# Optimization experiments

Measured on AMD Instinct MI355X. Metric: run time of the kernel, lower is better.

The kernel has to match this reference:

```python
import jax, jax.numpy as jnp
import numpy as np

D_MODEL, NUM_HEADS, ROPE_DIM = 256, 8, 16
B_GRAPHS, N_MAX = 16, 512


def _make_batch():
    # ragged graph sizes between 256 and 512 atoms; contiguous, sorted ids
    sizes = np.array([256 + (i * 256) // 15 for i in range(B_GRAPHS)], dtype=np.int64)
    return np.repeat(np.arange(B_GRAPHS), sizes)  # total N = 6137


def setup_inputs() -> dict:
    key = jax.random.key(0)
    ks = jax.random.split(key, 6)
    batch_np = _make_batch()
    N = int(batch_np.shape[0])
    x = jax.random.normal(ks[0], (N, D_MODEL), jnp.float32)
    pos = jax.random.normal(ks[1], (N, 3), jnp.float32) * 3.0
    W_qkv = jax.random.normal(ks[2], (D_MODEL, 3 * D_MODEL), jnp.float32) / np.sqrt(D_MODEL).astype(np.float32)
    W_out = jax.random.normal(ks[3], (D_MODEL, D_MODEL), jnp.float32) / np.sqrt(D_MODEL).astype(np.float32)
    rope_freqs = jax.random.normal(ks[4], (ROPE_DIM,), jnp.float32) * 0.1
    W_rope = jax.random.normal(ks[5], (ROPE_DIM, NUM_HEADS), jnp.float32) / np.sqrt(ROPE_DIM).astype(np.float32)
    gamma = jnp.ones((D_MODEL,), jnp.float32)
    beta = jnp.zeros((D_MODEL,), jnp.float32)
    return {"x": x, "pos": pos, "batch": jnp.asarray(batch_np, jnp.int32),
            "W_qkv": W_qkv, "W_out": W_out, "rope_freqs": rope_freqs,
            "W_rope": W_rope, "gamma": gamma, "beta": beta,
            "B": B_GRAPHS, "n_max": N_MAX}


def _forward(x, pos, W_qkv, W_out, rope_freqs, W_rope, gamma, beta, batch, B, n_max):
    N, d = x.shape
    H = W_rope.shape[1]
    hd = d // H
    scale = hd ** -0.5
    # pad ragged graphs to [B, n_max] via vectorized scatter (batch is sorted)
    sizes = jax.ops.segment_sum(jnp.ones((N,), jnp.int32), batch, num_segments=B)
    offsets = jnp.concatenate([jnp.zeros((1,), jnp.int32), jnp.cumsum(sizes)[:-1].astype(jnp.int32)])
    pidx = jnp.arange(N, dtype=jnp.int32) - offsets[batch]  # position within graph
    x_pad = jnp.zeros((B, n_max, d), x.dtype).at[batch, pidx].set(x)
    pos_pad = jnp.zeros((B, n_max, 3), pos.dtype).at[batch, pidx].set(pos)
    pad = jnp.ones((B, n_max), bool).at[batch, pidx].set(False)  # True = padding
    # multi-head self-attention on scalar channel
    qkv = x_pad @ W_qkv  # [B, n, 3d]
    q, k, v = jnp.split(qkv, 3, axis=-1)
    heads = lambda t: t.reshape(B, n_max, H, hd).transpose(0, 2, 1, 3)  # [B,H,n,hd]
    q, k, v = heads(q), heads(k), heads(v)
    logits = jnp.einsum('bhid,bhjd->bhij', q, k) * scale
    # Euclidean RoPE distance bias: rope_proj(cos(|omega| * ||r_i - r_j||))
    diff = pos_pad[:, :, None, :] - pos_pad[:, None, :, :]  # [B,n,n,3]
    sq = jnp.sum(diff * diff, axis=-1)
    dist = jnp.where(sq > 0, jnp.sqrt(jnp.where(sq > 0, sq, 1.0)), 0.0)  # safe norm
    fourier = jnp.cos(dist[..., None] * jnp.abs(rope_freqs))  # [B,n,n,r]
    bias = jnp.einsum('bijr,rh->bhij', fourier, W_rope)
    pair_pad = (pad[:, :, None] | pad[:, None, :])[:, None]  # [B,1,n,n]
    bias = jnp.where(pair_pad, 0.0, bias)
    logits = jnp.where(pad[:, None, None, :], -1e9, logits + bias)
    attn = jax.nn.softmax(logits, axis=-1)
    out = jnp.einsum('bhij,bhjd->bhid', attn, v)
    out = out.transpose(0, 2, 1, 3).reshape(B, n_max, d) @ W_out
    out_flat = out[batch, pidx]  # gather back to flat node list
    # residual + LayerNorm (eps = 1e-5)
    y = x + out_flat
    mu = jnp.mean(y, axis=-1, keepdims=True)
    var = jnp.mean((y - mu) ** 2, axis=-1, keepdims=True)
    return gamma * (y - mu) * jax.lax.rsqrt(var + 1e-5) + beta


def reference(x, pos, batch, W_qkv, W_out, rope_freqs, W_rope, gamma, beta, B, n_max):
    return _forward(x, pos, W_qkv, W_out, rope_freqs, W_rope, gamma, beta, batch, B, n_max)
```

## Files before the change

### kernel.cpp

```cpp
#include <hip/hip_runtime.h>
#include <hip/hip_bf16.h>

typedef __hip_bfloat16 bf16;
typedef short bf16x8 __attribute__((ext_vector_type(8)));
typedef float f32x4 __attribute__((ext_vector_type(4)));

#define NGRAPH 16
#define QSCALE 0.17677669529663687f
#define VT_LD 8192

struct __align__(16) bf8x { bf16 v[8]; };

__device__ __forceinline__ bf16x8 ldcvt8(const float* p) {
  float4 u = *(const float4*)p, v = *(const float4*)(p + 4);
  __align__(16) bf16 tmp[8];
  tmp[0] = __float2bfloat16(u.x); tmp[1] = __float2bfloat16(u.y);
  tmp[2] = __float2bfloat16(u.z); tmp[3] = __float2bfloat16(u.w);
  tmp[4] = __float2bfloat16(v.x); tmp[5] = __float2bfloat16(v.y);
  tmp[6] = __float2bfloat16(v.z); tmp[7] = __float2bfloat16(v.w);
  return *(const bf16x8*)tmp;
}

__global__ __launch_bounds__(256) void k_pre(const float* __restrict__ Wqkv,
                                             const float* __restrict__ Wout,
                                             const int* __restrict__ batch,
                                             bf16* __restrict__ Wqkv_t,
                                             bf16* __restrict__ Wout_t,
                                             int* __restrict__ offs, int N) {
  __shared__ float ld[64][65];
  int bid = blockIdx.x, t = threadIdx.x;
  int c = t & 63, r0 = t >> 6;
  if (bid < 48) {
    int k0 = (bid & 3) * 64, n0 = (bid >> 2) * 64;
    #pragma unroll
    for (int r = r0; r < 64; r += 4) ld[r][c] = Wqkv[(size_t)(k0 + r) * 768 + n0 + c];
    __syncthreads();
    #pragma unroll
    for (int r = r0; r < 64; r += 4)
      Wqkv_t[(size_t)(n0 + r) * 256 + k0 + c] = __float2bfloat16(ld[c][r]);
  } else if (bid < 64) {
    int b2 = bid - 48;
    int k0 = (b2 & 3) * 64, n0 = (b2 >> 2) * 64;
    #pragma unroll
    for (int r = r0; r < 64; r += 4) ld[r][c] = Wout[(size_t)(k0 + r) * 256 + n0 + c];
    __syncthreads();
    #pragma unroll
    for (int r = r0; r < 64; r += 4)
      Wout_t[(size_t)(n0 + r) * 256 + k0 + c] = __float2bfloat16(ld[c][r]);
  } else {
    for (int i = t; i < N; i += 256) {
      if (i == 0) { offs[0] = 0; offs[NGRAPH] = N; }
      else if (batch[i] != batch[i - 1]) offs[batch[i]] = i;
    }
  }
}

__global__ __launch_bounds__(256) void k_mid(const float* __restrict__ x,
                                             const bf16* __restrict__ Wqkv_t,
                                             const float* __restrict__ pos,
                                             const float* __restrict__ freqs,
                                             const float* __restrict__ Wrope,
                                             const int* __restrict__ batch,
                                             const int* __restrict__ offs,
                                             bf16* __restrict__ QKVb,
                                             bf16* __restrict__ VT,
                                             bf16* __restrict__ bias,
                                             int N, int MBm) {
  __shared__ __align__(16) char smem[18432];
  int t = threadIdx.x, bid = blockIdx.x;
  int nbg = MBm * 12;
  if (bid < nbg) {
    float (*tr)[65] = (float(*)[65])smem;
    int* rowcol = (int*)(smem + 16640);
    int w = t >> 6, l = t & 63, fr = l & 15, fq = l >> 4;
    int m0 = (bid % MBm) * 64, n0 = (bid / MBm) * 64;
    bool isV = (n0 >= 512);
    if (isV && t < 64) {
      int m = m0 + t; if (m > N - 1) m = N - 1;
      int b = batch[m];
      rowcol[t] = b * 512 + (m - offs[b]);
    }
    int arow = m0 + w * 16 + fr; if (arow > N - 1) arow = N - 1;
    bf16x8 af[8];
    #pragma unroll
    for (int kt = 0; kt < 8; ++kt)
      af[kt] = ldcvt8(x + (size_t)arow * 256 + kt * 32 + fq * 8);
    f32x4 acc[4];
    #pragma unroll
    for (int nt = 0; nt < 4; ++nt) acc[nt] = (f32x4){0.f, 0.f, 0.f, 0.f};
    #pragma unroll
    for (int nt = 0; nt < 4; ++nt) {
      int brow = n0 + nt * 16 + fr;
      #pragma unroll
      for (int kt = 0; kt < 8; ++kt) {
        bf16x8 bf_ = *(const bf16x8*)(Wqkv_t + (size_t)brow * 256 + kt * 32 + fq * 8);
        acc[nt] = __builtin_amdgcn_mfma_f32_16x16x32_bf16(af[kt], bf_, acc[nt], 0, 0, 0);
      }
    }
    #pragma unroll
    for (int nt = 0; nt < 4; ++nt) {
      int col = n0 + nt * 16 + fr;
      float sc = (col < 256) ? QSCALE : 1.f;
      #pragma unroll
      for (int rr = 0; rr < 4; ++rr) {
        int m = m0 + w * 16 + fq * 4 + rr;
        if (m < N) QKVb[(size_t)m * 768 + col] = __float2bfloat16(acc[nt][rr] * sc);
      }
    }
    if (isV) {
      #pragma unroll
      for (int nt = 0; nt < 4; ++nt)
        #pragma unroll
        for (int rr = 0; rr < 4; ++rr)
          tr[nt * 16 + fr][w * 16 + fq * 4 + rr] = acc[nt][rr];
      __syncthreads();
      int c = t >> 2, r0 = (t & 3) * 16;
      int dg = (n0 - 512) + c;
      #pragma unroll
      for (int i = 0; i < 16; ++i) {
        int r = r0 + i;
        VT[(size_t)dg * VT_LD + rowcol[r]] = __float2bfloat16(tr[c][r]);
      }
    }
  } else {
    float (*Sb)[16][36] = (float(*)[16][36])smem;
    int b2 = bid - nbg;
    int b = b2 >> 9;
    int q0 = (b2 & 31) * 16, j0 = ((b2 >> 5) & 15) * 32;
    int off = offs[b], n = offs[b + 1] - off;
    if (q0 >= n || j0 >= n) return;
    int tb = 0;
    for (int g = 0; g < b; ++g) {
      int ng = offs[g + 1] - offs[g];
      tb += ((ng + 15) >> 4) * ((ng + 31) >> 5);
    }
    int jtiles = (n + 31) >> 5;
    bf16* tile = bias + (size_t)(tb + (q0 >> 4) * jtiles + (j0 >> 5)) * 4096;
    int qs = t >> 5, j = t & 31;
    int jg = j0 + j; bool vj = jg < n;
    float jx, jy, jz;
    { int a = (vj ? off + jg : off) * 3; jx = pos[a]; jy = pos[a + 1]; jz = pos[a + 2]; }
    #pragma unroll
    for (int e = 0; e < 2; ++e) {
      int q = qs + 8 * e; int qg = q0 + q; bool vq = qg < n;
      float bv[8];
      #pragma unroll
      for (int h = 0; h < 8; ++h) bv[h] = 0.f;
      if (vq && vj) {
        int a = (off + qg) * 3;
        float dx = pos[a] - jx, dy = pos[a + 1] - jy, dz = pos[a + 2] - jz;
        float dist = sqrtf(dx * dx + dy * dy + dz * dz);
        #pragma unroll
        for (int r = 0; r < 16; ++r) {
          float cv = __cosf(dist * fabsf(freqs[r]));
          #pragma unroll
          for (int h = 0; h < 8; ++h) bv[h] += cv * Wrope[r * 8 + h];
        }
      }
      #pragma unroll
      for (int h = 0; h < 8; ++h) Sb[h][q][j] = (vq && vj) ? bv[h] : -1e30f;
    }
    __syncthreads();
    int w = t >> 6, l = t & 63, fq = l >> 4, fr = l & 15;
    #pragma unroll
    for (int hh = 0; hh < 2; ++hh) {
      int h = w * 2 + hh;
      __align__(16) bf16 pk[8];
      #pragma unroll
      for (int k = 0; k < 8; ++k)
        pk[k] = __float2bfloat16(Sb[h][fq * 4 + (k & 3)][(k >> 2) * 16 + fr]);
      *(bf16x8*)(tile + h * 512 + l * 8) = *(const bf16x8*)pk;
    }
  }
}

__global__ __launch_bounds__(256) void k_attn(const bf16* __restrict__ QKVb,
                                              const bf16* __restrict__ VT,
                                              const bf16* __restrict__ bias,
                                              const int* __restrict__ offs,
                                              bf16* __restrict__ Ob) {
  __shared__ __align__(16) bf16 Pt[4][16][40];
  int b = blockIdx.y, hbase = blockIdx.z * 4;
  int off = offs[b], n = offs[b + 1] - off;
  int q0 = blockIdx.x * 16;
  if (q0 >= n) return;
  int t = threadIdx.x, w = t >> 6, l = t & 63, fr = l & 15, fq = l >> 4;
  int h = hbase + w;
  int tb = 0;
  for (int g = 0; g < b; ++g) {
    int ng = offs[g + 1] - offs[g];
    tb += ((ng + 15) >> 4) * ((ng + 31) >> 5);
  }
  int jtiles = (n + 31) >> 5;
  const bf16* btile = bias + (size_t)(tb + (q0 >> 4) * jtiles) * 4096 + h * 512 + l * 8;
  const bf16* Kb = QKVb + (size_t)off * 768 + 256 + h * 32 + fq * 8;
  const bf16* Vb = VT + (size_t)(h * 32 + fr) * VT_LD + b * 512 + fq * 8;
  int qrow = q0 + fr; bool qv = qrow < n;
  bf16x8 aq = *(const bf16x8*)(QKVb + (size_t)(qv ? off + qrow : off) * 768 + h * 32 + fq * 8);
  if (!qv) aq = (bf16x8){0, 0, 0, 0, 0, 0, 0, 0};
  f32x4 Oa[2];
  Oa[0] = (f32x4){0.f, 0.f, 0.f, 0.f}; Oa[1] = (f32x4){0.f, 0.f, 0.f, 0.f};
  float lacc[4] = {0.f, 0.f, 0.f, 0.f};

#define LOADT(JT, B_, K0_, K1_, V0_, V1_) do {                                   \
    int _jt = (JT); int _k0 = _jt * 32 + fr, _k1 = _k0 + 16;                     \
    B_ = *(const bf8x*)(btile + (size_t)_jt * 4096);                             \
    K0_ = *(const bf16x8*)(Kb + (size_t)((_k0 < n) ? _k0 : 0) * 768);            \
    K1_ = *(const bf16x8*)(Kb + (size_t)((_k1 < n) ? _k1 : 0) * 768);            \
    V0_ = *(const bf16x8*)(Vb + _jt * 32);                                       \
    V1_ = *(const bf16x8*)(Vb + (size_t)16 * VT_LD + _jt * 32);                  \
  } while (0)

  bf8x cb; bf16x8 ck0, ck1, cv0, cv1;
  LOADT(0, cb, ck0, ck1, cv0, cv1);
  for (int jt = 0; jt < jtiles; ++jt) {
    bf8x nb; bf16x8 nk0, nk1, nv0, nv1;
    if (jt + 1 < jtiles) LOADT(jt + 1, nb, nk0, nk1, nv0, nv1);
    f32x4 z = {0.f, 0.f, 0.f, 0.f};
    f32x4 S0 = __builtin_amdgcn_mfma_f32_16x16x32_bf16(aq, ck0, z, 0, 0, 0);
    f32x4 S1 = __builtin_amdgcn_mfma_f32_16x16x32_bf16(aq, ck1, z, 0, 0, 0);
    #pragma unroll
    for (int k = 0; k < 8; ++k) {
      int jti = k >> 2, rr = k & 3;
      float s = (jti ? S1[rr] : S0[rr]) + __bfloat162float(cb.v[k]);
      float p = __expf(s);
      lacc[rr] += p;
      Pt[w][fq * 4 + rr][jti * 16 + fr] = __float2bfloat16(p);
    }
    bf16x8 ap = *(const bf16x8*)&Pt[w][fr][fq * 8];
    Oa[0] = __builtin_amdgcn_mfma_f32_16x16x32_bf16(ap, cv0, Oa[0], 0, 0, 0);
    Oa[1] = __builtin_amdgcn_mfma_f32_16x16x32_bf16(ap, cv1, Oa[1], 0, 0, 0);
    cb = nb; ck0 = nk0; ck1 = nk1; cv0 = nv0; cv1 = nv1;
  }
#undef LOADT
  #pragma unroll
  for (int rr = 0; rr < 4; ++rr) {
    #pragma unroll
    for (int m2 = 1; m2 <= 8; m2 <<= 1) lacc[rr] += __shfl_xor(lacc[rr], m2);
  }
  #pragma unroll
  for (int dh = 0; dh < 2; ++dh)
    #pragma unroll
    for (int rr = 0; rr < 4; ++rr) {
      int row = q0 + fq * 4 + rr;
      if (row < n)
        Ob[(size_t)(off + row) * 256 + h * 32 + dh * 16 + fr] =
            __float2bfloat16(Oa[dh][rr] / lacc[rr]);
    }
}

__global__ __launch_bounds__(256) void k_out_ln(const bf16* __restrict__ A,
                                                const bf16* __restrict__ Bt,
                                                const float* __restrict__ x,
                                                const float* __restrict__ gamma,
                                                const float* __restrict__ beta,
                                                float* __restrict__ out, int M) {
  __shared__ float ps[4][16], pss[4][16];
  int t = threadIdx.x, w = t >> 6, l = t & 63, fr = l & 15, fq = l >> 4;
  int m0 = blockIdx.x * 16;
  int arow = m0 + fr; if (arow > M - 1) arow = M - 1;
  bf16x8 af[8];
  #pragma unroll
  for (int kt = 0; kt < 8; ++kt)
    af[kt] = *(const bf16x8*)(A + (size_t)arow * 256 + kt * 32 + fq * 8);
  f32x4 acc[4];
  #pragma unroll
  for (int nt = 0; nt < 4; ++nt) {
    acc[nt] = (f32x4){0.f, 0.f, 0.f, 0.f};
    int brow = w * 64 + nt * 16 + fr;
    #pragma unroll
    for (int kt = 0; kt < 8; ++kt) {
      bf16x8 bf_ = *(const bf16x8*)(Bt + (size_t)brow * 256 + kt * 32 + fq * 8);
      acc[nt] = __builtin_amdgcn_mfma_f32_16x16x32_bf16(af[kt], bf_, acc[nt], 0, 0, 0);
    }
  }
  float y[4][4];
  #pragma unroll
  for (int rr = 0; rr < 4; ++rr) {
    int row = m0 + fq * 4 + rr;
    int rc = (row < M) ? row : (M - 1);
    float s = 0.f, ss = 0.f;
    #pragma unroll
    for (int nt = 0; nt < 4; ++nt) {
      float v = acc[nt][rr] + x[(size_t)rc * 256 + w * 64 + nt * 16 + fr];
      y[rr][nt] = v; s += v; ss += v * v;
    }
    #pragma unroll
    for (int m2 = 1; m2 <= 8; m2 <<= 1) { s += __shfl_xor(s, m2); ss += __shfl_xor(ss, m2); }
    if (fr == 0) { ps[w][fq * 4 + rr] = s; pss[w][fq * 4 + rr] = ss; }
  }
  __syncthreads();
  #pragma unroll
  for (int rr = 0; rr < 4; ++rr) {
    int row = m0 + fq * 4 + rr;
    int ri = fq * 4 + rr;
    float s = ps[0][ri] + ps[1][ri] + ps[2][ri] + ps[3][ri];
    float ss = pss[0][ri] + pss[1][ri] + pss[2][ri] + pss[3][ri];
    float mean = s * (1.f / 256.f);
    float var = ss * (1.f / 256.f) - mean * mean;
    float rstd = rsqrtf(var + 1e-5f);
    if (row < M) {
      #pragma unroll
      for (int nt = 0; nt < 4; ++nt) {
        int col = w * 64 + nt * 16 + fr;
        out[(size_t)row * 256 + col] = gamma[col] * (y[rr][nt] - mean) * rstd + beta[col];
      }
    }
  }
}

extern "C" void kernel_launch(void* const* d_in, const int* in_sizes, int n_in,
                              void* d_out, int out_size, void* d_ws, size_t ws_size,
                              hipStream_t stream) {
  (void)n_in; (void)out_size; (void)ws_size;
  const float* x     = (const float*)d_in[0];
  const float* pos   = (const float*)d_in[1];
  const int*   batch = (const int*)d_in[2];
  const float* Wqkv  = (const float*)d_in[3];
  const float* Wout  = (const float*)d_in[4];
  const float* freqs = (const float*)d_in[5];
  const float* Wrope = (const float*)d_in[6];
  const float* gamma = (const float*)d_in[7];
  const float* beta  = (const float*)d_in[8];
  float* out = (float*)d_out;

  int N = in_sizes[0] / 256;

  char* base = (char*)d_ws;
  int*   offs   = (int*)base;
  bf16*  QKVb   = (bf16*)(base + 1024);
  bf16*  VT     = (bf16*)(base + 9427456);
  bf16*  Wqkv_t = (bf16*)(base + 13621760);
  bf16*  Wout_t = (bf16*)(base + 14014976);
  bf16*  Ob     = (bf16*)(base + 14146048);
  bf16*  biasb  = (bf16*)(base + 17288192);

  int MBm = (N + 63) / 64;
  k_pre<<<65, 256, 0, stream>>>(Wqkv, Wout, batch, Wqkv_t, Wout_t, offs, N);
  k_mid<<<MBm * 12 + 8192, 256, 0, stream>>>(x, Wqkv_t, pos, freqs, Wrope, batch, offs,
                                             QKVb, VT, biasb, N, MBm);
  k_attn<<<dim3(32, NGRAPH, 2), 256, 0, stream>>>(QKVb, VT, biasb, offs, Ob);
  k_out_ln<<<(N + 15) / 16, 256, 0, stream>>>(Ob, Wout_t, x, gamma, beta, out, N);
}
```

Before: 182.2 us.

## Fuse RoPE distance bias computation into attention kernel, drop global bias buffer

Removes the bias-tile generation blocks from the mid kernel and computes the Fourier distance bias on the fly inside the attention kernel, double-buffered in shared memory per key tile. This eliminates writing and re-reading a large bf16 bias buffer through global memory and shrinks the GEMM launch. In exchange the cosine work is duplicated across the two head groups, and each loop iteration gains extra ALU work and a block-wide barrier.

Result: no change. 181.4 us (-0.4%).

```diff
diff --git a/kernel.cpp b/kernel.cpp
--- a/kernel.cpp
+++ b/kernel.cpp
@@ -8,8 +8,6 @@
 #define NGRAPH 16
 #define QSCALE 0.17677669529663687f
 #define VT_LD 8192
-
-struct __align__(16) bf8x { bf16 v[8]; };
 
 __device__ __forceinline__ bf16x8 ldcvt8(const float* p) {
   float4 u = *(const float4*)p, v = *(const float4*)(p + 4);
@@ -55,130 +53,76 @@
   }
 }
 
-__global__ __launch_bounds__(256) void k_mid(const float* __restrict__ x,
-                                             const bf16* __restrict__ Wqkv_t,
-                                             const float* __restrict__ pos,
-                                             const float* __restrict__ freqs,
-                                             const float* __restrict__ Wrope,
-                                             const int* __restrict__ batch,
-                                             const int* __restrict__ offs,
-                                             bf16* __restrict__ QKVb,
-                                             bf16* __restrict__ VT,
-                                             bf16* __restrict__ bias,
-                                             int N, int MBm) {
-  __shared__ __align__(16) char smem[18432];
+__global__ __launch_bounds__(256) void k_gemm(const float* __restrict__ x,
+                                              const bf16* __restrict__ Wqkv_t,
+                                              const int* __restrict__ batch,
+                                              const int* __restrict__ offs,
+                                              bf16* __restrict__ QKVb,
+                                              bf16* __restrict__ VT,
+                                              int N, int MBm) {
+  __shared__ float tr[64][65];
+  __shared__ int rowcol[64];
   int t = threadIdx.x, bid = blockIdx.x;
-  int nbg = MBm * 12;
-  if (bid < nbg) {
-    float (*tr)[65] = (float(*)[65])smem;
-    int* rowcol = (int*)(smem + 16640);
-    int w = t >> 6, l = t & 63, fr = l & 15, fq = l >> 4;
-    int m0 = (bid % MBm) * 64, n0 = (bid / MBm) * 64;
-    bool isV = (n0 >= 512);
-    if (isV && t < 64) {
-      int m = m0 + t; if (m > N - 1) m = N - 1;
-      int b = batch[m];
-      rowcol[t] = b * 512 + (m - offs[b]);
-    }
-    int arow = m0 + w * 16 + fr; if (arow > N - 1) arow = N - 1;
-    bf16x8 af[8];
-    #pragma unroll
-    for (int kt = 0; kt < 8; ++kt)
-      af[kt] = ldcvt8(x + (size_t)arow * 256 + kt * 32 + fq * 8);
-    f32x4 acc[4];
-    #pragma unroll
-    for (int nt = 0; nt < 4; ++nt) acc[nt] = (f32x4){0.f, 0.f, 0.f, 0.f};
-    #pragma unroll
-    for (int nt = 0; nt < 4; ++nt) {
-      int brow = n0 + nt * 16 + fr;
+  int w = t >> 6, l = t & 63, fr = l & 15, fq = l >> 4;
+  int m0 = (bid % MBm) * 64, n0 = (bid / MBm) * 64;
+  bool isV = (n0 >= 512);
+  if (isV && t < 64) {
+    int m = m0 + t; if (m > N - 1) m = N - 1;
+    int b = batch[m];
+    rowcol[t] = b * 512 + (m - offs[b]);
+  }
+  int arow = m0 + w * 16 + fr; if (arow > N - 1) arow = N - 1;
+  bf16x8 af[8];
+  #pragma unroll
+  for (int kt = 0; kt < 8; ++kt)
+    af[kt] = ldcvt8(x + (size_t)arow * 256 + kt * 32 + fq * 8);
+  f32x4 acc[4];
+  #pragma unroll
+  for (int nt = 0; nt < 4; ++nt) acc[nt] = (f32x4){0.f, 0.f, 0.f, 0.f};
+  #pragma unroll
+  for (int nt = 0; nt < 4; ++nt) {
+    int brow = n0 + nt * 16 + fr;
+    #pragma unroll
+    for (int kt = 0; kt < 8; ++kt) {
+      bf16x8 bf_ = *(const bf16x8*)(Wqkv_t + (size_t)brow * 256 + kt * 32 + fq * 8);
+      acc[nt] = __builtin_amdgcn_mfma_f32_16x16x32_bf16(af[kt], bf_, acc[nt], 0, 0, 0);
+    }
+  }
+  #pragma unroll
+  for (int nt = 0; nt < 4; ++nt) {
+    int col = n0 + nt * 16 + fr;
+    float sc = (col < 256) ? QSCALE : 1.f;
+    #pragma unroll
+    for (int rr = 0; rr < 4; ++rr) {
+      int m = m0 + w * 16 + fq * 4 + rr;
+      if (m < N) QKVb[(size_t)m * 768 + col] = __float2bfloat16(acc[nt][rr] * sc);
+    }
+  }
+  if (isV) {
+    #pragma unroll
+    for (int nt = 0; nt < 4; ++nt)
       #pragma unroll
-      for (int kt = 0; kt < 8; ++kt) {
-        bf16x8 bf_ = *(const bf16x8*)(Wqkv_t + (size_t)brow * 256 + kt * 32 + fq * 8);
-        acc[nt] = __builtin_amdgcn_mfma_f32_16x16x32_bf16(af[kt], bf_, acc[nt], 0, 0, 0);
-      }
-    }
-    #pragma unroll
-    for (int nt = 0; nt < 4; ++nt) {
-      int col = n0 + nt * 16 + fr;
-      float sc = (col < 256) ? QSCALE : 1.f;
-      #pragma unroll
-      for (int rr = 0; rr < 4; ++rr) {
-        int m = m0 + w * 16 + fq * 4 + rr;
-        if (m < N) QKVb[(size_t)m * 768 + col] = __float2bfloat16(acc[nt][rr] * sc);
-      }
-    }
-    if (isV) {
-      #pragma unroll
-      for (int nt = 0; nt < 4; ++nt)
-        #pragma unroll
-        for (int rr = 0; rr < 4; ++rr)
-          tr[nt * 16 + fr][w * 16 + fq * 4 + rr] = acc[nt][rr];
-      __syncthreads();
-      int c = t >> 2, r0 = (t & 3) * 16;
-      int dg = (n0 - 512) + c;
-      #pragma unroll
-      for (int i = 0; i < 16; ++i) {
-        int r = r0 + i;
-        VT[(size_t)dg * VT_LD + rowcol[r]] = __float2bfloat16(tr[c][r]);
-      }
-    }
-  } else {
-    float (*Sb)[16][36] = (float(*)[16][36])smem;
-    int b2 = bid - nbg;
-    int b = b2 >> 9;
-    int q0 = (b2 & 31) * 16, j0 = ((b2 >> 5) & 15) * 32;
-    int off = offs[b], n = offs[b + 1] - off;
-    if (q0 >= n || j0 >= n) return;
-    int tb = 0;
-    for (int g = 0; g < b; ++g) {
-      int ng = offs[g + 1] - offs[g];
-      tb += ((ng + 15) >> 4) * ((ng + 31) >> 5);
-    }
-    int jtiles = (n + 31) >> 5;
-    bf16* tile = bias + (size_t)(tb + (q0 >> 4) * jtiles + (j0 >> 5)) * 4096;
-    int qs = t >> 5, j = t & 31;
-    int jg = j0 + j; bool vj = jg < n;
-    float jx, jy, jz;
-    { int a = (vj ? off + jg : off) * 3; jx = pos[a]; jy = pos[a + 1]; jz = pos[a + 2]; }
-    #pragma unroll
-    for (int e = 0; e < 2; ++e) {
-      int q = qs + 8 * e; int qg = q0 + q; bool vq = qg < n;
-      float bv[8];
-      #pragma unroll
-      for (int h = 0; h < 8; ++h) bv[h] = 0.f;
-      if (vq && vj) {
-        int a = (off + qg) * 3;
-        float dx = pos[a] - jx, dy = pos[a + 1] - jy, dz = pos[a + 2] - jz;
-        float dist = sqrtf(dx * dx + dy * dy + dz * dz);
-        #pragma unroll
-        for (int r = 0; r < 16; ++r) {
-          float cv = __cosf(dist * fabsf(freqs[r]));
-          #pragma unroll
-          for (int h = 0; h < 8; ++h) bv[h] += cv * Wrope[r * 8 + h];
-        }
-      }
-      #pragma unroll
-      for (int h = 0; h < 8; ++h) Sb[h][q][j] = (vq && vj) ? bv[h] : -1e30f;
-    }
+      for (int rr = 0; rr < 4; ++rr)
+        tr[nt * 16 + fr][w * 16 + fq * 4 + rr] = acc[nt][rr];
     __syncthreads();
-    int w = t >> 6, l = t & 63, fq = l >> 4, fr = l & 15;
-    #pragma unroll
-    for (int hh = 0; hh < 2; ++hh) {
-      int h = w * 2 + hh;
-      __align__(16) bf16 pk[8];
-      #pragma unroll
-      for (int k = 0; k < 8; ++k)
-        pk[k] = __float2bfloat16(Sb[h][fq * 4 + (k & 3)][(k >> 2) * 16 + fr]);
-      *(bf16x8*)(tile + h * 512 + l * 8) = *(const bf16x8*)pk;
-    }
-  }
-}
-
-__global__ __launch_bounds__(256) void k_attn(const bf16* __restrict__ QKVb,
+    int c = t >> 2, r0 = (t & 3) * 16;
+    int dg = (n0 - 512) + c;
+    #pragma unroll
+    for (int i = 0; i < 16; ++i) {
+      int r = r0 + i;
+      VT[(size_t)dg * VT_LD + rowcol[r]] = __float2bfloat16(tr[c][r]);
+    }
+  }
+}
+
+__global__ __launch_bounds__(256) void k_attn(const float* __restrict__ pos,
+                                              const float* __restrict__ freqs,
+                                              const float* __restrict__ Wrope,
+                                              const bf16* __restrict__ QKVb,
                                               const bf16* __restrict__ VT,
-                                              const bf16* __restrict__ bias,
                                               const int* __restrict__ offs,
                                               bf16* __restrict__ Ob) {
+  __shared__ float Sb[2][4][16][36];
   __shared__ __align__(16) bf16 Pt[4][16][40];
   int b = blockIdx.y, hbase = blockIdx.z * 4;
   int off = offs[b], n = offs[b + 1] - off;
@@ -186,43 +130,79 @@
   if (q0 >= n) return;
   int t = threadIdx.x, w = t >> 6, l = t & 63, fr = l & 15, fq = l >> 4;
   int h = hbase + w;
-  int tb = 0;
-  for (int g = 0; g < b; ++g) {
-    int ng = offs[g + 1] - offs[g];
-    tb += ((ng + 15) >> 4) * ((ng + 31) >> 5);
-  }
-  int jtiles = (n + 31) >> 5;
-  const bf16* btile = bias + (size_t)(tb + (q0 >> 4) * jtiles) * 4096 + h * 512 + l * 8;
   const bf16* Kb = QKVb + (size_t)off * 768 + 256 + h * 32 + fq * 8;
   const bf16* Vb = VT + (size_t)(h * 32 + fr) * VT_LD + b * 512 + fq * 8;
   int qrow = q0 + fr; bool qv = qrow < n;
   bf16x8 aq = *(const bf16x8*)(QKVb + (size_t)(qv ? off + qrow : off) * 768 + h * 32 + fq * 8);
   if (!qv) aq = (bf16x8){0, 0, 0, 0, 0, 0, 0, 0};
+
+  int bq = t >> 5, bj = t & 31;
+  float qpx[2], qpy[2], qpz[2]; bool bqv[2];
+  #pragma unroll
+  for (int e = 0; e < 2; ++e) {
+    int qq = q0 + bq + 8 * e; bqv[e] = qq < n;
+    int a = (bqv[e] ? off + qq : off) * 3;
+    qpx[e] = pos[a]; qpy[e] = pos[a + 1]; qpz[e] = pos[a + 2];
+  }
+
   f32x4 Oa[2];
   Oa[0] = (f32x4){0.f, 0.f, 0.f, 0.f}; Oa[1] = (f32x4){0.f, 0.f, 0.f, 0.f};
   float lacc[4] = {0.f, 0.f, 0.f, 0.f};
-
-#define LOADT(JT, B_, K0_, K1_, V0_, V1_) do {                                   \
-    int _jt = (JT); int _k0 = _jt * 32 + fr, _k1 = _k0 + 16;                     \
-    B_ = *(const bf8x*)(btile + (size_t)_jt * 4096);                             \
-    K0_ = *(const bf16x8*)(Kb + (size_t)((_k0 < n) ? _k0 : 0) * 768);            \
-    K1_ = *(const bf16x8*)(Kb + (size_t)((_k1 < n) ? _k1 : 0) * 768);            \
-    V0_ = *(const bf16x8*)(Vb + _jt * 32);                                       \
-    V1_ = *(const bf16x8*)(Vb + (size_t)16 * VT_LD + _jt * 32);                  \
+  int jtiles = (n + 31) >> 5;
+
+#define PRODUCE(JT, BUF) do {                                                     \
+    int _jg = (JT) * 32 + bj; bool _vj = _jg < n;                                 \
+    int _a = (_vj ? off + _jg : off) * 3;                                         \
+    float _jx = pos[_a], _jy = pos[_a + 1], _jz = pos[_a + 2];                    \
+    _Pragma("unroll")                                                             \
+    for (int _e = 0; _e < 2; ++_e) {                                              \
+      float _b0 = 0.f, _b1 = 0.f, _b2 = 0.f, _b3 = 0.f;                           \
+      if (_vj && bqv[_e]) {                                                       \
+        float _dx = qpx[_e] - _jx, _dy = qpy[_e] - _jy, _dz = qpz[_e] - _jz;      \
+        float _d = sqrtf(_dx * _dx + _dy * _dy + _dz * _dz);                      \
+        _Pragma("unroll")                                                         \
+        for (int _r = 0; _r < 16; ++_r) {                                         \
+          float _cv = __cosf(_d * fabsf(freqs[_r]));                              \
+          _b0 += _cv * Wrope[_r * 8 + hbase + 0];                                 \
+          _b1 += _cv * Wrope[_r * 8 + hbase + 1];                                 \
+          _b2 += _cv * Wrope[_r * 8 + hbase + 2];                                 \
+          _b3 += _cv * Wrope[_r * 8 + hbase + 3];                                 \
+        }                                                                         \
+      }                                                                           \
+      int _qi = bq + 8 * _e;                                                      \
+      Sb[BUF][0][_qi][bj] = _vj ? _b0 : -1e30f;                                   \
+      Sb[BUF][1][_qi][bj] = _vj ? _b1 : -1e30f;                                   \
+      Sb[BUF][2][_qi][bj] = _vj ? _b2 : -1e30f;                                   \
+      Sb[BUF][3][_qi][bj] = _vj ? _b3 : -1e30f;                                   \
+    }                                                                             \
   } while (0)
 
-  bf8x cb; bf16x8 ck0, ck1, cv0, cv1;
-  LOADT(0, cb, ck0, ck1, cv0, cv1);
+#define LOADT(JT, K0_, K1_, V0_, V1_) do {                                        \
+    int _jt = (JT); int _k0 = _jt * 32 + fr, _k1 = _k0 + 16;                      \
+    K0_ = *(const bf16x8*)(Kb + (size_t)((_k0 < n) ? _k0 : 0) * 768);             \
+    K1_ = *(const bf16x8*)(Kb + (size_t)((_k1 < n) ? _k1 : 0) * 768);             \
+    V0_ = *(const bf16x8*)(Vb + _jt * 32);                                        \
+    V1_ = *(const bf16x8*)(Vb + (size_t)16 * VT_LD + _jt * 32);                   \
+  } while (0)
+
+  bf16x8 ck0, ck1, cv0, cv1;
+  LOADT(0, ck0, ck1, cv0, cv1);
+  PRODUCE(0, 0);
+  __syncthreads();
   for (int jt = 0; jt < jtiles; ++jt) {
-    bf8x nb; bf16x8 nk0, nk1, nv0, nv1;
-    if (jt + 1 < jtiles) LOADT(jt + 1, nb, nk0, nk1, nv0, nv1);
+    int par = jt & 1;
+    bf16x8 nk0, nk1, nv0, nv1;
+    if (jt + 1 < jtiles) {
+      LOADT(jt + 1, nk0, nk1, nv0, nv1);
+      PRODUCE(jt + 1, par ^ 1);
+    }
     f32x4 z = {0.f, 0.f, 0.f, 0.f};
     f32x4 S0 = __builtin_amdgcn_mfma_f32_16x16x32_bf16(aq, ck0, z, 0, 0, 0);
     f32x4 S1 = __builtin_amdgcn_mfma_f32_16x16x32_bf16(aq, ck1, z, 0, 0, 0);
     #pragma unroll
     for (int k = 0; k < 8; ++k) {
       int jti = k >> 2, rr = k & 3;
-      float s = (jti ? S1[rr] : S0[rr]) + __bfloat162float(cb.v[k]);
+      float s = (jti ? S1[rr] : S0[rr]) + Sb[par][w][fq * 4 + rr][jti * 16 + fr];
       float p = __expf(s);
       lacc[rr] += p;
       Pt[w][fq * 4 + rr][jti * 16 + fr] = __float2bfloat16(p);
@@ -230,9 +210,11 @@
     bf16x8 ap = *(const bf16x8*)&Pt[w][fr][fq * 8];
     Oa[0] = __builtin_amdgcn_mfma_f32_16x16x32_bf16(ap, cv0, Oa[0], 0, 0, 0);
     Oa[1] = __builtin_amdgcn_mfma_f32_16x16x32_bf16(ap, cv1, Oa[1], 0, 0, 0);
-    cb = nb; ck0 = nk0; ck1 = nk1; cv0 = nv0; cv1 = nv1;
+    ck0 = nk0; ck1 = nk1; cv0 = nv0; cv1 = nv1;
+    __syncthreads();
   }
 #undef LOADT
+#undef PRODUCE
   #pragma unroll
   for (int rr = 0; rr < 4; ++rr) {
     #pragma unroll
@@ -333,12 +315,10 @@
   bf16*  Wqkv_t = (bf16*)(base + 13621760);
   bf16*  Wout_t = (bf16*)(base + 14014976);
   bf16*  Ob     = (bf16*)(base + 14146048);
-  bf16*  biasb  = (bf16*)(base + 17288192);
 
   int MBm = (N + 63) / 64;
   k_pre<<<65, 256, 0, stream>>>(Wqkv, Wout, batch, Wqkv_t, Wout_t, offs, N);
-  k_mid<<<MBm * 12 + 8192, 256, 0, stream>>>(x, Wqkv_t, pos, freqs, Wrope, batch, offs,
-                                             QKVb, VT, biasb, N, MBm);
-  k_attn<<<dim3(32, NGRAPH, 2), 256, 0, stream>>>(QKVb, VT, biasb, offs, Ob);
+  k_gemm<<<MBm * 12, 256, 0, stream>>>(x, Wqkv_t, batch, offs, QKVb, VT, N, MBm);
+  k_attn<<<dim3(32, NGRAPH, 2), 256, 0, stream>>>(pos, freqs, Wrope, QKVb, VT, offs, Ob);
   k_out_ln<<<(N + 15) / 16, 256, 0, stream>>>(Ob, Wout_t, x, gamma, beta, out, N);
 }
```
